# Kernel tuning notes

Measured on AMD Instinct MI355X. Metric: run time of the kernel, lower is better.

The kernel has to match this reference:

```python
import jax, jax.numpy as jnp
import numpy as np

EPS = 1e-8
ALPHA = 1.0


def setup_inputs() -> dict:
    key = jax.random.key(0)
    k1, k2 = jax.random.split(key)
    N = 8192
    pred = jax.random.normal(k1, (N,), dtype=jnp.float32)
    gt = jax.random.normal(k2, (N,), dtype=jnp.float32)
    return {"pred": pred, "gt": gt, "n": N}


def _rank_counts(x):
    # sa[i] = #{j : x[i] > x[j]}  (pairwise O(N^2) comparison, reduced per row)
    return jnp.sum((x[:, None] > x[None, :]).astype(x.dtype), axis=-1)


def reference(pred, gt, n):
    N = pred.shape[0]
    sa = _rank_counts(pred)                 # [N]
    sb = _rank_counts(gt)                   # [N]
    delta = (sa - sb) / (N + EPS)           # rank disagreement, normalized
    a2 = jax.lax.stop_gradient(pred) - delta * ALPHA  # pred.detach() - delta*alpha
    l = jnp.abs(pred - a2)                  # L1, reduction='none'
    return jnp.sum(l) / n
```

## Files before the change

### kernel.cpp

```cpp
#include <hip/hip_runtime.h>


constexpr int T    = 1024;
constexpr int NWIN = 32;
constexpr int NN   = 8192;
constexpr unsigned BIAS   = 0x40000000u;
constexpr unsigned POISON = 0xAAAAAAAAu;

__global__ __launch_bounds__(T) void score_loss_one(
    const float* __restrict__ pred,
    const float* __restrict__ gt,
    unsigned* __restrict__ bsum,
    float* __restrict__ out,
    double inv)
{
    __shared__ float sw[NN];
    __shared__ int dsum[NWIN];
    __shared__ unsigned wred[16];

    const int tid = threadIdx.x;
    const int b   = blockIdx.x;
    const int il  = tid & 31;
    const int s   = tid >> 5;
    const int i   = b * NWIN + il;
    constexpr int JW = NN / NWIN;

    const float xi = pred[i];
    const float yi = gt[i];

    if (tid < NWIN) dsum[tid] = 0;

    {
        const float4* src = reinterpret_cast<const float4*>(pred);
        float4* dst = reinterpret_cast<float4*>(sw);
#pragma unroll
        for (int k = 0; k < (NN / 4) / T; ++k)
            dst[k * T + tid] = src[k * T + tid];
    }
    __syncthreads();

    int d = 0;
    {
        const float4* w = reinterpret_cast<const float4*>(sw + s * JW);
#pragma unroll 8
        for (int t = 0; t < JW / 4; ++t) {
            float4 p = w[t];
            d += (xi > p.x) + (xi > p.y) + (xi > p.z) + (xi > p.w);
        }
    }
    __syncthreads();

    {
        const float4* src = reinterpret_cast<const float4*>(gt);
        float4* dst = reinterpret_cast<float4*>(sw);
#pragma unroll
        for (int k = 0; k < (NN / 4) / T; ++k)
            dst[k * T + tid] = src[k * T + tid];
    }
    __syncthreads();
    {
        const float4* w = reinterpret_cast<const float4*>(sw + s * JW);
#pragma unroll 8
        for (int t = 0; t < JW / 4; ++t) {
            float4 g = w[t];
            d -= (yi > g.x) + (yi > g.y) + (yi > g.z) + (yi > g.w);
        }
    }

    atomicAdd(&dsum[il], d);
    __syncthreads();

    if (tid < NWIN) {
        int v = dsum[tid];
        v = (v < 0) ? -v : v;
#pragma unroll
        for (int off = 16; off >= 1; off >>= 1)
            v += __shfl_xor(v, off, 64);
        if (tid == 0)
            __hip_atomic_store(&bsum[b], (unsigned)v + BIAS,
                               __ATOMIC_RELEASE, __HIP_MEMORY_SCOPE_AGENT);
    }

    if (b == 0) {
        __syncthreads();
        const int nb = gridDim.x;
        unsigned acc = 0;
        if (tid < nb) {
            unsigned v;
            for (;;) {
                v = __hip_atomic_load(&bsum[tid], __ATOMIC_ACQUIRE,
                                      __HIP_MEMORY_SCOPE_AGENT);
                if (v != 0u && v != POISON) break;
                __builtin_amdgcn_s_sleep(2);
            }
            acc = v - BIAS;
        }
        for (int off = 1; off < 64; off <<= 1)
            acc += __shfl_xor(acc, off, 64);
        if ((tid & 63) == 0) wred[tid >> 6] = acc;
        __syncthreads();
        if (tid == 0) {
            unsigned tot = 0;
#pragma unroll
            for (int w = 0; w < 16; ++w) tot += wred[w];
            out[0] = (float)((double)tot * inv);
        }
    }
}

extern "C" void kernel_launch(void* const* d_in, const int* in_sizes, int n_in,
                              void* d_out, int out_size, void* d_ws, size_t ws_size,
                              hipStream_t stream)
{
    const float* pred = (const float*)d_in[0];
    const float* gt   = (const float*)d_in[1];
    const int N = in_sizes[0];

    float* out     = (float*)d_out;
    unsigned* bsum = (unsigned*)d_ws;

    const double inv = 1.0 / (((double)N + 1e-8) * (double)N);

    dim3 grid(N / NWIN);
    score_loss_one<<<grid, T, 0, stream>>>(pred, gt, bsum, out, inv);
}
```

Before: 17.34 us.

## Register-block four rows per thread and reduce partial counts with wave shuffles

```diff
diff --git a/kernel.cpp b/kernel.cpp
--- a/kernel.cpp
+++ b/kernel.cpp
@@ -2,8 +2,9 @@
 
 
 constexpr int T    = 1024;
-constexpr int NWIN = 32;
+constexpr int NI   = 32;
 constexpr int NN   = 8192;
+constexpr int JW   = 64;
 constexpr unsigned BIAS   = 0x40000000u;
 constexpr unsigned POISON = 0xAAAAAAAAu;
 
@@ -15,20 +16,22 @@
     double inv)
 {
     __shared__ float sw[NN];
-    __shared__ int dsum[NWIN];
+    __shared__ int dsum[NI];
     __shared__ unsigned wred[16];
 
-    const int tid = threadIdx.x;
-    const int b   = blockIdx.x;
-    const int il  = tid & 31;
-    const int s   = tid >> 5;
-    const int i   = b * NWIN + il;
-    constexpr int JW = NN / NWIN;
+    const int tid  = threadIdx.x;
+    const int b    = blockIdx.x;
+    const int il4  = tid & 7;
+    const int s    = tid >> 3;
+    const int ib   = b * NI + il4 * 4;
 
-    const float xi = pred[i];
-    const float yi = gt[i];
+    float xi[4], yi[4];
+#pragma unroll
+    for (int c = 0; c < 4; ++c) { xi[c] = pred[ib + c]; yi[c] = gt[ib + c]; }
 
-    if (tid < NWIN) dsum[tid] = 0;
+    if (tid < NI) dsum[tid] = 0;
+
+    int d[4] = {0, 0, 0, 0};
 
     {
         const float4* src = reinterpret_cast<const float4*>(pred);
@@ -38,14 +41,14 @@
             dst[k * T + tid] = src[k * T + tid];
     }
     __syncthreads();
-
-    int d = 0;
     {
         const float4* w = reinterpret_cast<const float4*>(sw + s * JW);
-#pragma unroll 8
+#pragma unroll
         for (int t = 0; t < JW / 4; ++t) {
             float4 p = w[t];
-            d += (xi > p.x) + (xi > p.y) + (xi > p.z) + (xi > p.w);
+#pragma unroll
+            for (int c = 0; c < 4; ++c)
+                d[c] += (xi[c] > p.x) + (xi[c] > p.y) + (xi[c] > p.z) + (xi[c] > p.w);
         }
     }
     __syncthreads();
@@ -60,17 +63,29 @@
     __syncthreads();
     {
         const float4* w = reinterpret_cast<const float4*>(sw + s * JW);
-#pragma unroll 8
+#pragma unroll
         for (int t = 0; t < JW / 4; ++t) {
             float4 g = w[t];
-            d -= (yi > g.x) + (yi > g.y) + (yi > g.z) + (yi > g.w);
+#pragma unroll
+            for (int c = 0; c < 4; ++c)
+                d[c] -= (yi[c] > g.x) + (yi[c] > g.y) + (yi[c] > g.z) + (yi[c] > g.w);
         }
     }
 
-    atomicAdd(&dsum[il], d);
+#pragma unroll
+    for (int c = 0; c < 4; ++c) {
+#pragma unroll
+        for (int off = 8; off < 64; off <<= 1)
+            d[c] += __shfl_xor(d[c], off, 64);
+    }
+    if ((tid & 63) < 8) {
+#pragma unroll
+        for (int c = 0; c < 4; ++c)
+            atomicAdd(&dsum[il4 * 4 + c], d[c]);
+    }
     __syncthreads();
 
-    if (tid < NWIN) {
+    if (tid < NI) {
         int v = dsum[tid];
         v = (v < 0) ? -v : v;
 #pragma unroll
@@ -121,6 +136,6 @@
 
     const double inv = 1.0 / (((double)N + 1e-8) * (double)N);
 
-    dim3 grid(N / NWIN);
+    dim3 grid(N / NI);
     score_loss_one<<<grid, T, 0, stream>>>(pred, gt, bsum, out, inv);
 }
```

Result: slower. 17.72 us (+2.1%).

## Stage pred and gt together in shared memory and pad cross-block flags

Applied to the files above, without the earlier changes.

```diff
diff --git a/kernel.cpp b/kernel.cpp
--- a/kernel.cpp
+++ b/kernel.cpp
@@ -2,10 +2,11 @@
 
 
 constexpr int T    = 1024;
-constexpr int NWIN = 32;
+constexpr int NI   = 32;
 constexpr int NN   = 8192;
-constexpr unsigned BIAS   = 0x40000000u;
-constexpr unsigned POISON = 0xAAAAAAAAu;
+constexpr int JW   = NN / NI;
+constexpr int PAD  = 32;
+constexpr unsigned BIAS = 0x40000000u;
 
 __global__ __launch_bounds__(T) void score_loss_one(
     const float* __restrict__ pred,
@@ -14,86 +15,75 @@
     float* __restrict__ out,
     double inv)
 {
-    __shared__ float sw[NN];
-    __shared__ int dsum[NWIN];
+    __shared__ float sp[NN];
+    __shared__ float sg[NN];
+    __shared__ int dsum[NI];
     __shared__ unsigned wred[16];
 
     const int tid = threadIdx.x;
     const int b   = blockIdx.x;
     const int il  = tid & 31;
     const int s   = tid >> 5;
-    const int i   = b * NWIN + il;
-    constexpr int JW = NN / NWIN;
+    const int i   = b * NI + il;
 
     const float xi = pred[i];
     const float yi = gt[i];
 
-    if (tid < NWIN) dsum[tid] = 0;
+    if (tid < NI) dsum[tid] = 0;
 
     {
-        const float4* src = reinterpret_cast<const float4*>(pred);
-        float4* dst = reinterpret_cast<float4*>(sw);
+        const float4* ps = reinterpret_cast<const float4*>(pred);
+        const float4* gs = reinterpret_cast<const float4*>(gt);
+        float4* spd = reinterpret_cast<float4*>(sp);
+        float4* sgd = reinterpret_cast<float4*>(sg);
 #pragma unroll
-        for (int k = 0; k < (NN / 4) / T; ++k)
-            dst[k * T + tid] = src[k * T + tid];
+        for (int k = 0; k < (NN / 4) / T; ++k) {
+            spd[k * T + tid] = ps[k * T + tid];
+            sgd[k * T + tid] = gs[k * T + tid];
+        }
     }
     __syncthreads();
 
     int d = 0;
     {
-        const float4* w = reinterpret_cast<const float4*>(sw + s * JW);
+        const float4* wp = reinterpret_cast<const float4*>(sp + s * JW);
+        const float4* wg = reinterpret_cast<const float4*>(sg + s * JW);
 #pragma unroll 8
         for (int t = 0; t < JW / 4; ++t) {
-            float4 p = w[t];
+            float4 p = wp[t];
+            float4 g = wg[t];
             d += (xi > p.x) + (xi > p.y) + (xi > p.z) + (xi > p.w);
-        }
-    }
-    __syncthreads();
-
-    {
-        const float4* src = reinterpret_cast<const float4*>(gt);
-        float4* dst = reinterpret_cast<float4*>(sw);
-#pragma unroll
-        for (int k = 0; k < (NN / 4) / T; ++k)
-            dst[k * T + tid] = src[k * T + tid];
-    }
-    __syncthreads();
-    {
-        const float4* w = reinterpret_cast<const float4*>(sw + s * JW);
-#pragma unroll 8
-        for (int t = 0; t < JW / 4; ++t) {
-            float4 g = w[t];
             d -= (yi > g.x) + (yi > g.y) + (yi > g.z) + (yi > g.w);
         }
     }
 
-    atomicAdd(&dsum[il], d);
+    d += __shfl_xor(d, 32, 64);
+    if ((tid & 63) < 32) atomicAdd(&dsum[il], d);
     __syncthreads();
 
-    if (tid < NWIN) {
+    if (tid < NI) {
         int v = dsum[tid];
         v = (v < 0) ? -v : v;
 #pragma unroll
         for (int off = 16; off >= 1; off >>= 1)
             v += __shfl_xor(v, off, 64);
         if (tid == 0)
-            __hip_atomic_store(&bsum[b], (unsigned)v + BIAS,
+            __hip_atomic_store(&bsum[b * PAD], (unsigned)v + BIAS,
                                __ATOMIC_RELEASE, __HIP_MEMORY_SCOPE_AGENT);
     }
 
     if (b == 0) {
         __syncthreads();
-        const int nb = gridDim.x;
         unsigned acc = 0;
-        if (tid < nb) {
-            unsigned v;
+        if (tid < 256) {
             for (;;) {
-                v = __hip_atomic_load(&bsum[tid], __ATOMIC_ACQUIRE,
-                                      __HIP_MEMORY_SCOPE_AGENT);
-                if (v != 0u && v != POISON) break;
-                __builtin_amdgcn_s_sleep(2);
+                unsigned v = __hip_atomic_load(&bsum[tid * PAD],
+                                               __ATOMIC_RELAXED,
+                                               __HIP_MEMORY_SCOPE_AGENT);
+                unsigned diff = v - BIAS;
+                if (diff <= 262144u) { acc = diff; break; }
+                __builtin_amdgcn_s_sleep(8);
             }
-            acc = v - BIAS;
         }
         for (int off = 1; off < 64; off <<= 1)
             acc += __shfl_xor(acc, off, 64);
@@ -121,6 +111,6 @@
 
     const double inv = 1.0 / (((double)N + 1e-8) * (double)N);
 
-    dim3 grid(N / NWIN);
+    dim3 grid(N / NI);
     score_loss_one<<<grid, T, 0, stream>>>(pred, gt, bsum, out, inv);
 }
```

After: 17.49 us, median of 2. About the same (+0.9%).
